# Kernel tuning notes

Measured on AMD Instinct MI355X. Metric: run time of the kernel, lower is better.

## Reference

```python
import jax, jax.numpy as jnp
import numpy as np

V = 50000   # num_candidates
D = 32      # dim_item
B = 4096    # batch
N = 16      # max_n_node
L = 20      # max_session_length
STEPS = 1   # propagation_steps


def setup_inputs() -> dict:
    key = jax.random.key(0)
    ks = jax.random.split(key, 19)
    s = 1.0 / np.sqrt(D)
    u = lambda k, shp: jax.random.uniform(k, shp, jnp.float32, -s, s)
    return {
        "alias_inputs": jax.random.randint(ks[0], (B, L), 0, N),
        "A": jax.random.uniform(ks[1], (B, N, 2 * N), jnp.float32),
        "items": jax.random.randint(ks[2], (B, N), 0, V),
        "mask": jnp.ones((B, L), jnp.int32),
        "emb": u(ks[3], (V, D)),
        "w_ih": u(ks[4], (3 * D, 2 * D)),
        "w_hh": u(ks[5], (3 * D, D)),
        "b_ih": u(ks[6], (3 * D,)),
        "b_hh": u(ks[7], (3 * D,)),
        "b_iah": u(ks[8], (D,)),
        "b_oah": u(ks[9], (D,)),
        "w_ein": u(ks[10], (D, D)),
        "b_ein": u(ks[11], (D,)),
        "w_eout": u(ks[12], (D, D)),
        "b_eout": u(ks[13], (D,)),
        "w1": u(ks[14], (D, D)),
        "b1": u(ks[15], (D,)),
        "w2": u(ks[16], (D, D)),
        "b2": u(ks[17], (D,)),
        "w3": u(ks[18], (D, 1)),
    }


def reference(alias_inputs, A, items, mask, emb, w_ih, w_hh, b_ih, b_hh,
              b_iah, b_oah, w_ein, b_ein, w_eout, b_eout, w1, b1, w2, b2, w3):
    # item embedding lookup: [B, N, D]
    h = emb[items]
    n = A.shape[1]
    for _ in range(STEPS):
        node_in = h @ w_ein + b_ein
        node_out = h @ w_eout + b_eout
        # adjacency message passing (incoming / outgoing halves of A)
        input_in = jnp.matmul(A[:, :, :n], node_in) + b_iah
        input_out = jnp.matmul(A[:, :, n:2 * n], node_out) + b_oah
        inputs = jnp.concatenate([input_in, input_out], axis=-1)  # [B,N,2D]
        gi = inputs @ w_ih.T + b_ih   # [B,N,3D]
        gh = h @ w_hh.T + b_hh        # [B,N,3D]
        i_r, i_i, i_n = jnp.split(gi, 3, axis=-1)
        h_r, h_i, h_n = jnp.split(gh, 3, axis=-1)
        resetgate = jax.nn.sigmoid(i_r + h_r)
        inputgate = jax.nn.sigmoid(i_i + h_i)
        newgate = jnp.tanh(i_n + resetgate * h_n)
        h = newgate + inputgate * (h - newgate)
    # per-sample gather: seq_hidden[b, t] = h[b, alias_inputs[b, t]]
    seq = jnp.take_along_axis(h, alias_inputs[:, :, None], axis=1)  # [B,L,D]
    last = jnp.sum(mask, axis=1) - 1
    ht = seq[jnp.arange(seq.shape[0]), last]  # [B,D]
    q1 = (ht @ w1 + b1)[:, None, :]           # [B,1,D]
    q2 = seq @ w2 + b2                        # [B,L,D]
    alpha = jax.nn.sigmoid(q1 + q2) @ w3      # [B,L,1]
    s_g = jnp.sum(alpha * seq * mask[:, :, None].astype(seq.dtype), axis=1)
    scores = s_g @ emb[1:].T                  # [B, V-1]
    return scores
```

## Files before the change

kernel.cpp:

```cpp
#include <hip/hip_runtime.h>
#include <hip/hip_bf16.h>


#define B_BATCH 4096
#define N_NODE  16
#define L_SEQ   20
#define D_DIM   32
#define NV_OUT  49999
#define EMB_ROWS 50176

typedef float  f32x4  __attribute__((ext_vector_type(4)));
typedef float  f32x4u __attribute__((ext_vector_type(4), aligned(4)));
typedef __bf16 bf16x8 __attribute__((ext_vector_type(8)));

__device__ __forceinline__ float sigf(float x) {
    return 1.0f / (1.0f + __expf(-x));
}

__global__ __launch_bounds__(256) void session3_kernel(
    const int*   __restrict__ alias_inputs,
    const float* __restrict__ A,
    const int*   __restrict__ items,
    const int*   __restrict__ mask,
    const float* __restrict__ emb,
    const float* __restrict__ w_ih,
    const float* __restrict__ w_hh,
    const float* __restrict__ b_ih, const float* __restrict__ b_hh,
    const float* __restrict__ b_iah, const float* __restrict__ b_oah,
    const float* __restrict__ w_ein, const float* __restrict__ b_ein,
    const float* __restrict__ w_eout, const float* __restrict__ b_eout,
    const float* __restrict__ w1, const float* __restrict__ b1,
    const float* __restrict__ w2, const float* __restrict__ b2,
    const float* __restrict__ w3,
    float* __restrict__ sg_out)
{
    const int b   = blockIdx.x;
    const int tid = threadIdx.x;
    const int g   = tid >> 5;
    const int d   = tid & 31;
    const int n0  = g, n1 = g + 8;

    __shared__ float h_s [N_NODE][D_DIM];
    __shared__ float A_s [N_NODE][2 * N_NODE];
    __shared__ float ni_s[N_NODE][D_DIM];
    __shared__ float no_s[N_NODE][D_DIM];
    __shared__ float ii_s[N_NODE][D_DIM];
    __shared__ float io_s[N_NODE][D_DIM];
    __shared__ float wih_s[96][66];
    __shared__ float whh_s[96][34];
    __shared__ float q1_s[D_DIM];
    __shared__ float alpha_s[L_SEQ];
    __shared__ int   last_s;

    for (int idx = tid; idx < 512; idx += 256) {
        const int n = idx >> 5, dd = idx & 31;
        const int it = items[b * N_NODE + n];
        h_s[n][dd] = emb[(size_t)it * D_DIM + dd];
        A_s[n][dd] = A[(size_t)b * 512 + idx];
    }
    for (int f = tid; f < 96 * 64; f += 256) wih_s[f >> 6][f & 63] = w_ih[f];
    for (int f = tid; f < 96 * 32; f += 256) whh_s[f >> 5][f & 31] = w_hh[f];
    __syncthreads();

    float ai0 = b_ein[d], ao0 = b_eout[d];
    float ai1 = ai0,      ao1 = ao0;
    #pragma unroll
    for (int k = 0; k < 32; ++k) {
        const float we = w_ein[k * 32 + d], wo = w_eout[k * 32 + d];
        const float h0 = h_s[n0][k], h1 = h_s[n1][k];
        ai0 += h0 * we; ai1 += h1 * we;
        ao0 += h0 * wo; ao1 += h1 * wo;
    }
    ni_s[n0][d] = ai0; ni_s[n1][d] = ai1;
    no_s[n0][d] = ao0; no_s[n1][d] = ao1;
    __syncthreads();

    float iv0 = b_iah[d], ov0 = b_oah[d];
    float iv1 = iv0,      ov1 = ov0;
    #pragma unroll
    for (int m = 0; m < N_NODE; ++m) {
        const float nim = ni_s[m][d], nom = no_s[m][d];
        iv0 += A_s[n0][m]          * nim;
        iv1 += A_s[n1][m]          * nim;
        ov0 += A_s[n0][N_NODE + m] * nom;
        ov1 += A_s[n1][N_NODE + m] * nom;
    }
    ii_s[n0][d] = iv0; ii_s[n1][d] = iv1;
    io_s[n0][d] = ov0; io_s[n1][d] = ov1;
    __syncthreads();

    float r0 = b_ih[d] + b_hh[d],           r1 = r0;
    float i0 = b_ih[32 + d] + b_hh[32 + d], i1 = i0;
    float gn0 = b_ih[64 + d],               gn1 = gn0;
    float hn0 = b_hh[64 + d],               hn1 = hn0;
    #pragma unroll
    for (int k = 0; k < 32; ++k) {
        const float wri = wih_s[d][k],      wro = wih_s[d][32 + k];
        const float wii = wih_s[32 + d][k], wio = wih_s[32 + d][32 + k];
        const float wni = wih_s[64 + d][k], wno = wih_s[64 + d][32 + k];
        const float whr = whh_s[d][k];
        const float whi = whh_s[32 + d][k];
        const float whn = whh_s[64 + d][k];
        const float a0 = ii_s[n0][k], a1 = ii_s[n1][k];
        const float o0 = io_s[n0][k], o1 = io_s[n1][k];
        const float h0 = h_s[n0][k],  h1 = h_s[n1][k];
        r0  += a0 * wri + o0 * wro + h0 * whr;
        r1  += a1 * wri + o1 * wro + h1 * whr;
        i0  += a0 * wii + o0 * wio + h0 * whi;
        i1  += a1 * wii + o1 * wio + h1 * whi;
        gn0 += a0 * wni + o0 * wno;
        gn1 += a1 * wni + o1 * wno;
        hn0 += h0 * whn;
        hn1 += h1 * whn;
    }

    float hv0, hv1;
    {
        const float rg0 = sigf(r0), ig0 = sigf(i0);
        const float x0  = gn0 + rg0 * hn0;
        const float e0  = __expf(2.0f * fabsf(x0));
        const float ng0 = copysignf(1.0f - 2.0f / (e0 + 1.0f), x0);
        hv0 = ng0 + ig0 * (h_s[n0][d] - ng0);
        const float rg1 = sigf(r1), ig1 = sigf(i1);
        const float x1  = gn1 + rg1 * hn1;
        const float e1  = __expf(2.0f * fabsf(x1));
        const float ng1 = copysignf(1.0f - 2.0f / (e1 + 1.0f), x1);
        hv1 = ng1 + ig1 * (h_s[n1][d] - ng1);
    }
    __syncthreads();
    h_s[n0][d] = hv0;
    h_s[n1][d] = hv1;
    __syncthreads();

    for (int idx = tid; idx < L_SEQ * D_DIM; idx += 256) {
        const int t = idx >> 5, dd = idx & 31;
        const int a = alias_inputs[b * L_SEQ + t];
        const float v = h_s[a][dd];
        if (t < 16) ni_s[t][dd] = v;
        else        no_s[t - 16][dd] = v;
    }
    if (tid == 0) {
        int s = 0;
        for (int t = 0; t < L_SEQ; ++t) s += mask[b * L_SEQ + t];
        last_s = s - 1;
    }
    __syncthreads();

    if (tid < D_DIM) {
        const int lt = last_s;
        const float* sl = (lt < 16) ? &ni_s[lt][0] : &no_s[lt - 16][0];
        float acc = b1[tid];
        #pragma unroll
        for (int k = 0; k < 32; ++k) acc += sl[k] * w1[k * 32 + tid];
        q1_s[tid] = acc;
    }
    __syncthreads();

    for (int idx = tid; idx < L_SEQ * D_DIM; idx += 256) {
        const int t = idx >> 5, dd = idx & 31;
        const float* sp = (t < 16) ? &ni_s[t][0] : &no_s[t - 16][0];
        float q2 = b2[dd];
        #pragma unroll
        for (int k = 0; k < 32; ++k) q2 += sp[k] * w2[k * 32 + dd];
        const float val = sigf(q1_s[dd] + q2) * w3[dd];
        if (t < 16) ii_s[t][dd] = val;
        else        io_s[t - 16][dd] = val;
    }
    __syncthreads();
    if (tid < L_SEQ) {
        const float* tp = (tid < 16) ? &ii_s[tid][0] : &io_s[tid - 16][0];
        float a = 0.0f;
        #pragma unroll
        for (int dd = 0; dd < 32; ++dd) a += tp[dd];
        alpha_s[tid] = a * (float)mask[b * L_SEQ + tid];
    }
    __syncthreads();

    if (tid < D_DIM) {
        float acc = 0.0f;
        #pragma unroll
        for (int t = 0; t < L_SEQ; ++t) {
            const float sv = (t < 16) ? ni_s[t][tid] : no_s[t - 16][tid];
            acc += alpha_s[t] * sv;
        }
        sg_out[b * D_DIM + tid] = acc;
    }
}

__global__ __launch_bounds__(256) void conv_emb_kernel(
    const float* __restrict__ emb, __hip_bfloat16* __restrict__ emb_b)
{
    const int total = EMB_ROWS * D_DIM;
    for (int i = blockIdx.x * 256 + threadIdx.x; i < total; i += gridDim.x * 256) {
        const int v = i >> 5, k = i & 31;
        int src = v + 1;
        if (src > NV_OUT) src = NV_OUT;
        emb_b[i] = __float2bfloat16(emb[(size_t)src * D_DIM + k]);
    }
}

__global__ __launch_bounds__(256) void conv_sg_kernel(
    const float* __restrict__ sg,
    __hip_bfloat16* __restrict__ hi, __hip_bfloat16* __restrict__ lo)
{
    const int i = blockIdx.x * 256 + threadIdx.x;
    const float x = sg[i];
    const __hip_bfloat16 h = __float2bfloat16(x);
    hi[i] = h;
    lo[i] = __float2bfloat16(x - __bfloat162float(h));
}

__global__ __launch_bounds__(256) void score8_kernel(
    const __hip_bfloat16* __restrict__ sg_hi,
    const __hip_bfloat16* __restrict__ sg_lo,
    const __hip_bfloat16* __restrict__ emb_b,
    float* __restrict__ out)
{
    __shared__ float T[16][260];
    const int wave = threadIdx.x >> 6;
    const int lane = threadIdx.x & 63;
    const int rc   = lane & 15;
    const int kgrp = lane >> 4;
    const int b0   = blockIdx.y * 16;
    const int v0   = blockIdx.x * 256;
    const int vw   = v0 + wave * 64;

    const bf16x8 ah = *reinterpret_cast<const bf16x8*>(
        &sg_hi[(size_t)(b0 + rc) * D_DIM + kgrp * 8]);
    const bf16x8 al = *reinterpret_cast<const bf16x8*>(
        &sg_lo[(size_t)(b0 + rc) * D_DIM + kgrp * 8]);

    #pragma unroll
    for (int s = 0; s < 4; ++s) {
        const int vt = vw + s * 16;
        const bf16x8 bf = *reinterpret_cast<const bf16x8*>(
            &emb_b[(size_t)(vt + rc) * D_DIM + kgrp * 8]);
        f32x4 acc = {0.0f, 0.0f, 0.0f, 0.0f};
        acc = __builtin_amdgcn_mfma_f32_16x16x32_bf16(ah, bf, acc, 0, 0, 0);
        acc = __builtin_amdgcn_mfma_f32_16x16x32_bf16(al, bf, acc, 0, 0, 0);
        const int col = wave * 64 + s * 16 + rc;
        #pragma unroll
        for (int j = 0; j < 4; ++j)
            T[kgrp * 4 + j][col] = acc[j];
    }
    __syncthreads();

    if (v0 + 256 <= NV_OUT) {
        #pragma unroll
        for (int r = 0; r < 4; ++r) {
            const int row = wave * 4 + r;
            const f32x4 val = *reinterpret_cast<const f32x4*>(&T[row][lane * 4]);
            f32x4u* op = reinterpret_cast<f32x4u*>(
                &out[(size_t)(b0 + row) * NV_OUT + v0 + lane * 4]);
            __builtin_nontemporal_store(val, op);
        }
    } else {
        #pragma unroll
        for (int r = 0; r < 4; ++r) {
            const int row = wave * 4 + r;
            float* op = &out[(size_t)(b0 + row) * NV_OUT];
            #pragma unroll
            for (int j = 0; j < 4; ++j) {
                const int c = lane * 4 + j;
                if (v0 + c < NV_OUT) op[v0 + c] = T[row][c];
            }
        }
    }
}

extern "C" void kernel_launch(void* const* d_in, const int* in_sizes, int n_in,
                              void* d_out, int out_size, void* d_ws, size_t ws_size,
                              hipStream_t stream)
{
    const int*   alias_inputs = (const int*)  d_in[0];
    const float* A      = (const float*)d_in[1];
    const int*   items  = (const int*)  d_in[2];
    const int*   mask   = (const int*)  d_in[3];
    const float* emb    = (const float*)d_in[4];
    const float* w_ih   = (const float*)d_in[5];
    const float* w_hh   = (const float*)d_in[6];
    const float* b_ih   = (const float*)d_in[7];
    const float* b_hh   = (const float*)d_in[8];
    const float* b_iah  = (const float*)d_in[9];
    const float* b_oah  = (const float*)d_in[10];
    const float* w_ein  = (const float*)d_in[11];
    const float* b_ein  = (const float*)d_in[12];
    const float* w_eout = (const float*)d_in[13];
    const float* b_eout = (const float*)d_in[14];
    const float* w1     = (const float*)d_in[15];
    const float* b1     = (const float*)d_in[16];
    const float* w2     = (const float*)d_in[17];
    const float* b2     = (const float*)d_in[18];
    const float* w3     = (const float*)d_in[19];

    float* sg = (float*)d_ws;
    __hip_bfloat16* sg_hi = (__hip_bfloat16*)((char*)d_ws + 512 * 1024);
    __hip_bfloat16* sg_lo = (__hip_bfloat16*)((char*)d_ws + 768 * 1024);
    __hip_bfloat16* emb_b = (__hip_bfloat16*)((char*)d_ws + 1024 * 1024);
    float* out = (float*)d_out;

    hipLaunchKernelGGL(conv_emb_kernel, dim3(2048), dim3(256), 0, stream,
                       emb, emb_b);

    hipLaunchKernelGGL(session3_kernel, dim3(B_BATCH), dim3(256), 0, stream,
                       alias_inputs, A, items, mask, emb,
                       w_ih, w_hh, b_ih, b_hh, b_iah, b_oah,
                       w_ein, b_ein, w_eout, b_eout,
                       w1, b1, w2, b2, w3, sg);

    hipLaunchKernelGGL(conv_sg_kernel, dim3(B_BATCH * D_DIM / 256), dim3(256),
                       0, stream, sg, sg_hi, sg_lo);

    hipLaunchKernelGGL(score8_kernel,
                       dim3((NV_OUT + 255) / 256, B_BATCH / 16),
                       dim3(256), 0, stream, sg_hi, sg_lo, emb_b, out);
}
```

Before: 316.6 us.

## Double batch rows per score block, vectorize LDS reads, drop nontemporal stores

The score kernel now handles 32 batch rows per block instead of 16. Each emb tile fetched from memory is reused for two MFMA pairs, and the grid y dimension is halved. Output stores switch from nontemporal to regular stores. The session kernel's inner loops now read h, A and the intermediate activations from shared memory as float4 vectors, cutting LDS instruction count. The bigger LDS tile lowers occupancy, and regular stores may pollute the cache while writing the roughly 800 MB output.

```diff
diff --git a/kernel.cpp b/kernel.cpp
--- a/kernel.cpp
+++ b/kernel.cpp
@@ -65,11 +65,17 @@
     float ai0 = b_ein[d], ao0 = b_eout[d];
     float ai1 = ai0,      ao1 = ao0;
     #pragma unroll
-    for (int k = 0; k < 32; ++k) {
-        const float we = w_ein[k * 32 + d], wo = w_eout[k * 32 + d];
-        const float h0 = h_s[n0][k], h1 = h_s[n1][k];
-        ai0 += h0 * we; ai1 += h1 * we;
-        ao0 += h0 * wo; ao1 += h1 * wo;
+    for (int kb = 0; kb < 8; ++kb) {
+        const int k0 = kb * 4;
+        const f32x4 h0v = *reinterpret_cast<const f32x4*>(&h_s[n0][k0]);
+        const f32x4 h1v = *reinterpret_cast<const f32x4*>(&h_s[n1][k0]);
+        #pragma unroll
+        for (int j = 0; j < 4; ++j) {
+            const int k = k0 + j;
+            const float we = w_ein[k * 32 + d], wo = w_eout[k * 32 + d];
+            ai0 += h0v[j] * we; ai1 += h1v[j] * we;
+            ao0 += h0v[j] * wo; ao1 += h1v[j] * wo;
+        }
     }
     ni_s[n0][d] = ai0; ni_s[n1][d] = ai1;
     no_s[n0][d] = ao0; no_s[n1][d] = ao1;
@@ -78,12 +84,21 @@
     float iv0 = b_iah[d], ov0 = b_oah[d];
     float iv1 = iv0,      ov1 = ov0;
     #pragma unroll
-    for (int m = 0; m < N_NODE; ++m) {
-        const float nim = ni_s[m][d], nom = no_s[m][d];
-        iv0 += A_s[n0][m]          * nim;
-        iv1 += A_s[n1][m]          * nim;
-        ov0 += A_s[n0][N_NODE + m] * nom;
-        ov1 += A_s[n1][N_NODE + m] * nom;
+    for (int mb = 0; mb < 4; ++mb) {
+        const int m0 = mb * 4;
+        const f32x4 a0i = *reinterpret_cast<const f32x4*>(&A_s[n0][m0]);
+        const f32x4 a1i = *reinterpret_cast<const f32x4*>(&A_s[n1][m0]);
+        const f32x4 a0o = *reinterpret_cast<const f32x4*>(&A_s[n0][N_NODE + m0]);
+        const f32x4 a1o = *reinterpret_cast<const f32x4*>(&A_s[n1][N_NODE + m0]);
+        #pragma unroll
+        for (int j = 0; j < 4; ++j) {
+            const int m = m0 + j;
+            const float nim = ni_s[m][d], nom = no_s[m][d];
+            iv0 += a0i[j] * nim;
+            iv1 += a1i[j] * nim;
+            ov0 += a0o[j] * nom;
+            ov1 += a1o[j] * nom;
+        }
     }
     ii_s[n0][d] = iv0; ii_s[n1][d] = iv1;
     io_s[n0][d] = ov0; io_s[n1][d] = ov1;
@@ -94,24 +109,32 @@
     float gn0 = b_ih[64 + d],               gn1 = gn0;
     float hn0 = b_hh[64 + d],               hn1 = hn0;
     #pragma unroll
-    for (int k = 0; k < 32; ++k) {
-        const float wri = wih_s[d][k],      wro = wih_s[d][32 + k];
-        const float wii = wih_s[32 + d][k], wio = wih_s[32 + d][32 + k];
-        const float wni = wih_s[64 + d][k], wno = wih_s[64 + d][32 + k];
-        const float whr = whh_s[d][k];
-        const float whi = whh_s[32 + d][k];
-        const float whn = whh_s[64 + d][k];
-        const float a0 = ii_s[n0][k], a1 = ii_s[n1][k];
-        const float o0 = io_s[n0][k], o1 = io_s[n1][k];
-        const float h0 = h_s[n0][k],  h1 = h_s[n1][k];
-        r0  += a0 * wri + o0 * wro + h0 * whr;
-        r1  += a1 * wri + o1 * wro + h1 * whr;
-        i0  += a0 * wii + o0 * wio + h0 * whi;
-        i1  += a1 * wii + o1 * wio + h1 * whi;
-        gn0 += a0 * wni + o0 * wno;
-        gn1 += a1 * wni + o1 * wno;
-        hn0 += h0 * whn;
-        hn1 += h1 * whn;
+    for (int kb = 0; kb < 8; ++kb) {
+        const int k0 = kb * 4;
+        const f32x4 a0v = *reinterpret_cast<const f32x4*>(&ii_s[n0][k0]);
+        const f32x4 a1v = *reinterpret_cast<const f32x4*>(&ii_s[n1][k0]);
+        const f32x4 o0v = *reinterpret_cast<const f32x4*>(&io_s[n0][k0]);
+        const f32x4 o1v = *reinterpret_cast<const f32x4*>(&io_s[n1][k0]);
+        const f32x4 h0v = *reinterpret_cast<const f32x4*>(&h_s[n0][k0]);
+        const f32x4 h1v = *reinterpret_cast<const f32x4*>(&h_s[n1][k0]);
+        #pragma unroll
+        for (int j = 0; j < 4; ++j) {
+            const int k = k0 + j;
+            const float wri = wih_s[d][k],      wro = wih_s[d][32 + k];
+            const float wii = wih_s[32 + d][k], wio = wih_s[32 + d][32 + k];
+            const float wni = wih_s[64 + d][k], wno = wih_s[64 + d][32 + k];
+            const float whr = whh_s[d][k];
+            const float whi = whh_s[32 + d][k];
+            const float whn = whh_s[64 + d][k];
+            r0  += a0v[j] * wri + o0v[j] * wro + h0v[j] * whr;
+            r1  += a1v[j] * wri + o1v[j] * wro + h1v[j] * whr;
+            i0  += a0v[j] * wii + o0v[j] * wio + h0v[j] * whi;
+            i1  += a1v[j] * wii + o1v[j] * wio + h1v[j] * whi;
+            gn0 += a0v[j] * wni + o0v[j] * wno;
+            gn1 += a1v[j] * wni + o1v[j] * wno;
+            hn0 += h0v[j] * whn;
+            hn1 += h1v[j] * whn;
+        }
     }
 
     float hv0, hv1;
@@ -210,54 +233,62 @@
     lo[i] = __float2bfloat16(x - __bfloat162float(h));
 }
 
-__global__ __launch_bounds__(256) void score8_kernel(
+__global__ __launch_bounds__(256) void score9_kernel(
     const __hip_bfloat16* __restrict__ sg_hi,
     const __hip_bfloat16* __restrict__ sg_lo,
     const __hip_bfloat16* __restrict__ emb_b,
     float* __restrict__ out)
 {
-    __shared__ float T[16][260];
+    __shared__ float T[32][260];
     const int wave = threadIdx.x >> 6;
     const int lane = threadIdx.x & 63;
     const int rc   = lane & 15;
     const int kgrp = lane >> 4;
-    const int b0   = blockIdx.y * 16;
+    const int b0   = blockIdx.y * 32;
     const int v0   = blockIdx.x * 256;
     const int vw   = v0 + wave * 64;
 
-    const bf16x8 ah = *reinterpret_cast<const bf16x8*>(
+    const bf16x8 ah0 = *reinterpret_cast<const bf16x8*>(
         &sg_hi[(size_t)(b0 + rc) * D_DIM + kgrp * 8]);
-    const bf16x8 al = *reinterpret_cast<const bf16x8*>(
+    const bf16x8 al0 = *reinterpret_cast<const bf16x8*>(
         &sg_lo[(size_t)(b0 + rc) * D_DIM + kgrp * 8]);
+    const bf16x8 ah1 = *reinterpret_cast<const bf16x8*>(
+        &sg_hi[(size_t)(b0 + 16 + rc) * D_DIM + kgrp * 8]);
+    const bf16x8 al1 = *reinterpret_cast<const bf16x8*>(
+        &sg_lo[(size_t)(b0 + 16 + rc) * D_DIM + kgrp * 8]);
 
     #pragma unroll
     for (int s = 0; s < 4; ++s) {
         const int vt = vw + s * 16;
         const bf16x8 bf = *reinterpret_cast<const bf16x8*>(
             &emb_b[(size_t)(vt + rc) * D_DIM + kgrp * 8]);
-        f32x4 acc = {0.0f, 0.0f, 0.0f, 0.0f};
-        acc = __builtin_amdgcn_mfma_f32_16x16x32_bf16(ah, bf, acc, 0, 0, 0);
-        acc = __builtin_amdgcn_mfma_f32_16x16x32_bf16(al, bf, acc, 0, 0, 0);
+        f32x4 acc0 = {0.0f, 0.0f, 0.0f, 0.0f};
+        acc0 = __builtin_amdgcn_mfma_f32_16x16x32_bf16(ah0, bf, acc0, 0, 0, 0);
+        acc0 = __builtin_amdgcn_mfma_f32_16x16x32_bf16(al0, bf, acc0, 0, 0, 0);
+        f32x4 acc1 = {0.0f, 0.0f, 0.0f, 0.0f};
+        acc1 = __builtin_amdgcn_mfma_f32_16x16x32_bf16(ah1, bf, acc1, 0, 0, 0);
+        acc1 = __builtin_amdgcn_mfma_f32_16x16x32_bf16(al1, bf, acc1, 0, 0, 0);
         const int col = wave * 64 + s * 16 + rc;
         #pragma unroll
-        for (int j = 0; j < 4; ++j)
-            T[kgrp * 4 + j][col] = acc[j];
+        for (int j = 0; j < 4; ++j) {
+            T[kgrp * 4 + j][col]      = acc0[j];
+            T[16 + kgrp * 4 + j][col] = acc1[j];
+        }
     }
     __syncthreads();
 
     if (v0 + 256 <= NV_OUT) {
         #pragma unroll
-        for (int r = 0; r < 4; ++r) {
-            const int row = wave * 4 + r;
+        for (int r = 0; r < 8; ++r) {
+            const int row = wave * 8 + r;
             const f32x4 val = *reinterpret_cast<const f32x4*>(&T[row][lane * 4]);
-            f32x4u* op = reinterpret_cast<f32x4u*>(
-                &out[(size_t)(b0 + row) * NV_OUT + v0 + lane * 4]);
-            __builtin_nontemporal_store(val, op);
+            *reinterpret_cast<f32x4u*>(
+                &out[(size_t)(b0 + row) * NV_OUT + v0 + lane * 4]) = val;
         }
     } else {
         #pragma unroll
-        for (int r = 0; r < 4; ++r) {
-            const int row = wave * 4 + r;
+        for (int r = 0; r < 8; ++r) {
+            const int row = wave * 8 + r;
             float* op = &out[(size_t)(b0 + row) * NV_OUT];
             #pragma unroll
             for (int j = 0; j < 4; ++j) {
@@ -311,7 +342,7 @@
     hipLaunchKernelGGL(conv_sg_kernel, dim3(B_BATCH * D_DIM / 256), dim3(256),
                        0, stream, sg, sg_hi, sg_lo);
 
-    hipLaunchKernelGGL(score8_kernel,
-                       dim3((NV_OUT + 255) / 256, B_BATCH / 16),
+    hipLaunchKernelGGL(score9_kernel,
+                       dim3((NV_OUT + 255) / 256, B_BATCH / 32),
                        dim3(256), 0, stream, sg_hi, sg_lo, emb_b, out);
 }
```

New measurement: 333.1 us. 1.05x slower.
